# Kernel optimization log

Hardware: AMD Instinct MI355X
Metric: run time of the kernel (lower is better)

## Reference

```python
import jax, jax.numpy as jnp
import numpy as np

N_NODES = 50000
N_EDGES = 800000
N_GRAPHS = 64
IN_DIM, HID, OUT = 128, 128, 16


def gcn_conv(x, src, dst, deg_inv_sqrt, W, b):
    # x: [N, Cin]; src/dst: [E+N] (self-loops appended); W: [Cin, Cout]
    h = x @ W                                   # [N, Cout]
    norm = deg_inv_sqrt[src] * deg_inv_sqrt[dst]  # [E+N]
    msg = h[src] * norm[:, None]                # gather + scale
    out = jax.ops.segment_sum(msg, dst, num_segments=N_NODES)
    return out + b


def setup_inputs() -> dict:
    key = jax.random.key(0)
    ks = jax.random.split(key, 8)
    x = jax.random.normal(ks[0], (N_NODES, IN_DIM), dtype=jnp.float32)
    edge_index = jax.random.randint(ks[1], (2, N_EDGES), 0, N_NODES, dtype=jnp.int64)
    batch = jnp.sort(jax.random.randint(ks[2], (N_NODES,), 0, N_GRAPHS, dtype=jnp.int64))
    s = 1.0 / np.sqrt(IN_DIM)
    W1 = jax.random.normal(ks[3], (IN_DIM, HID), dtype=jnp.float32) * s
    b1 = jnp.zeros((HID,), dtype=jnp.float32)
    W2 = jax.random.normal(ks[4], (HID, HID), dtype=jnp.float32) * (1.0 / np.sqrt(HID))
    b2 = jnp.zeros((HID,), dtype=jnp.float32)
    Wfc = jax.random.normal(ks[5], (HID, OUT), dtype=jnp.float32) * (1.0 / np.sqrt(HID))
    bfc = jnp.zeros((OUT,), dtype=jnp.float32)
    return {"x": x, "edge_index": edge_index, "batch": batch,
            "W1": W1, "b1": b1, "W2": W2, "b2": b2, "Wfc": Wfc, "bfc": bfc}


def reference(x, edge_index, batch, W1, b1, W2, b2, Wfc, bfc):
    self_loops = jnp.arange(N_NODES, dtype=edge_index.dtype)
    src = jnp.concatenate([edge_index[0], self_loops])  # [E+N]
    dst = jnp.concatenate([edge_index[1], self_loops])
    deg = jax.ops.segment_sum(jnp.ones_like(dst, dtype=x.dtype), dst, num_segments=N_NODES)
    deg_inv_sqrt = jnp.where(deg > 0, jax.lax.rsqrt(deg), 0.0)

    h = jax.nn.relu(gcn_conv(x, src, dst, deg_inv_sqrt, W1, b1))
    h = jax.nn.relu(gcn_conv(h, src, dst, deg_inv_sqrt, W2, b2))

    # global mean pool over graphs
    sums = jax.ops.segment_sum(h, batch, num_segments=N_GRAPHS)         # [G, HID]
    cnts = jax.ops.segment_sum(jnp.ones((N_NODES,), h.dtype), batch, num_segments=N_GRAPHS)
    pooled = sums / jnp.maximum(cnts, 1.0)[:, None]

    return pooled @ Wfc + bfc  # [G, OUT]
```

## Files before the change

### kernel.cpp

```cpp
#include <hip/hip_runtime.h>
#include <math.h>

#define N_NODES 50000
#define N_EDGES 800000
#define N_GRAPHS 64
#define DIM 128
#define OUTD 16

#define BSHIFT 8
#define BNODES 256
#define NBUCK ((N_NODES + BNODES - 1) / BNODES)
#define TILE 2048
#define RCAP 8192
#define BSLOT 4864
#define GEMMB 256
#define BIN_GRID ((N_EDGES + TILE - 1) / TILE)

typedef __attribute__((ext_vector_type(8))) short short8;
typedef __attribute__((ext_vector_type(4))) float f32x4;

static __device__ __forceinline__ unsigned short f2bf(float f) {
    unsigned u = __float_as_uint(f);
    u += 0x7fffu + ((u >> 16) & 1u);
    return (unsigned short)(u >> 16);
}
static __device__ __forceinline__ float bfl(unsigned u) {
    return __uint_as_float(u << 16);
}
static __device__ __forceinline__ float bfh(unsigned u) {
    return __uint_as_float(u & 0xffff0000u);
}

__global__ __launch_bounds__(256) void k_init(int* __restrict__ bcnt,
                                              float* __restrict__ pool,
                                              const float* __restrict__ W2,
                                              unsigned* __restrict__ W2f) {
    int tid = threadIdx.x;
    if (tid < NBUCK) bcnt[tid] = 0;
    for (int i = tid; i < N_GRAPHS * DIM; i += 256) pool[i] = 0.f;
    for (int idx = tid; idx < (DIM / 2) * DIM; idx += 256) {
        int kp = idx >> 7;
        int n  = idx & 127;
        int k  = kp * 2;
        int kstep = kp >> 4;
        int quad  = (kp >> 2) & 3;
        int jw    = kp & 3;
        int ct    = n >> 4;
        unsigned vlo = f2bf(W2[(size_t)k * DIM + n]);
        unsigned vhi = f2bf(W2[(size_t)(k + 1) * DIM + n]);
        W2f[(((kstep * 8 + ct) * 64) + quad * 16 + (n & 15)) * 4 + jw] = vlo | (vhi << 16);
    }
}

template <int BF16IN>
static __device__ __forceinline__ void gemm_body(const void* __restrict__ Av,
                                                 const float* __restrict__ Wg,
                                                 unsigned short* __restrict__ C,
                                                 int nrows,
                                                 unsigned* smemW, unsigned* smemC,
                                                 int tile0, int tstride) {
    unsigned* Wl = smemW;
    {
        int t = threadIdx.x;
        int p = t & 63;
        int kp = p * 2;
        int n0 = (t >> 6) * 32;
        int kstep = kp >> 5;
        int quad = (kp >> 3) & 3;
        int jw = (kp & 7) >> 1;
        const float* r0 = Wg + (size_t)kp * DIM;
        const float* r1 = r0 + DIM;
        int rot = (p >> 2) & 7;
#pragma unroll
        for (int i4 = 0; i4 < 8; ++i4) {
            int nb = ((i4 + rot) & 7) * 4;
            int n = n0 + nb;
            float4 lo = *(const float4*)(r0 + n);
            float4 hi = *(const float4*)(r1 + n);
            const float* lp = &lo.x;
            const float* hp = &hi.x;
#pragma unroll
            for (int ii = 0; ii < 4; ++ii) {
                int nn = n + ii;
                int ct = nn >> 4;
                int l  = quad * 16 + (nn & 15);
                unsigned vlo = f2bf(lp[ii]);
                unsigned vhi = f2bf(hp[ii]);
                Wl[(((kstep * 8 + ct) * 64) + l) * 4 + jw] = vlo | (vhi << 16);
            }
        }
    }
    __syncthreads();

    int wid  = threadIdx.x >> 6;
    int lane = threadIdx.x & 63;
    int m    = lane & 15;
    int quad = lane >> 4;
    const short8* Wf = (const short8*)Wl;
    unsigned short* cs = (unsigned short*)smemC + wid * 4352;
    const unsigned char* cb = (const unsigned char*)smemC + wid * 8704;

    int ntiles = (nrows + 127) / 128;
    for (int tile = tile0; tile < ntiles; tile += tstride) {
        int row0 = tile * 128 + wid * 32;
        if (row0 >= nrows) continue;

        int rA = row0 + m;      if (rA >= nrows) rA = nrows - 1;
        int rB = row0 + 16 + m; if (rB >= nrows) rB = nrows - 1;

        short8 af0[4], af1[4];
        if (BF16IN) {
            const unsigned short* arowA = (const unsigned short*)Av + (size_t)rA * DIM + quad * 8;
            const unsigned short* arowB = (const unsigned short*)Av + (size_t)rB * DIM + quad * 8;
#pragma unroll
            for (int ks = 0; ks < 4; ++ks) {
                af0[ks] = *(const short8*)(arowA + ks * 32);
                af1[ks] = *(const short8*)(arowB + ks * 32);
            }
        } else {
            const float* arowA = (const float*)Av + (size_t)rA * DIM + quad * 8;
            const float* arowB = (const float*)Av + (size_t)rB * DIM + quad * 8;
#pragma unroll
            for (int ks = 0; ks < 4; ++ks) {
                float4 lo = *(const float4*)(arowA + ks * 32);
                float4 hi = *(const float4*)(arowA + ks * 32 + 4);
                short8 f;
                f[0] = (short)f2bf(lo.x); f[1] = (short)f2bf(lo.y);
                f[2] = (short)f2bf(lo.z); f[3] = (short)f2bf(lo.w);
                f[4] = (short)f2bf(hi.x); f[5] = (short)f2bf(hi.y);
                f[6] = (short)f2bf(hi.z); f[7] = (short)f2bf(hi.w);
                af0[ks] = f;
                lo = *(const float4*)(arowB + ks * 32);
                hi = *(const float4*)(arowB + ks * 32 + 4);
                f[0] = (short)f2bf(lo.x); f[1] = (short)f2bf(lo.y);
                f[2] = (short)f2bf(lo.z); f[3] = (short)f2bf(lo.w);
                f[4] = (short)f2bf(hi.x); f[5] = (short)f2bf(hi.y);
                f[6] = (short)f2bf(hi.z); f[7] = (short)f2bf(hi.w);
                af1[ks] = f;
            }
        }

        f32x4 acc0[8], acc1[8];
#pragma unroll
        for (int ct = 0; ct < 8; ++ct) {
            acc0[ct] = (f32x4){0.f, 0.f, 0.f, 0.f};
            acc1[ct] = (f32x4){0.f, 0.f, 0.f, 0.f};
        }

#pragma unroll
        for (int ks = 0; ks < 4; ++ks) {
#pragma unroll
            for (int ct = 0; ct < 8; ++ct) {
                short8 bfrag = Wf[(ks * 8 + ct) * 64 + lane];
                acc0[ct] = __builtin_amdgcn_mfma_f32_16x16x32_bf16(af0[ks], bfrag, acc0[ct], 0, 0, 0);
                acc1[ct] = __builtin_amdgcn_mfma_f32_16x16x32_bf16(af1[ks], bfrag, acc1[ct], 0, 0, 0);
            }
        }

#pragma unroll
        for (int ct = 0; ct < 8; ++ct) {
#pragma unroll
            for (int reg = 0; reg < 4; ++reg) {
                cs[(quad * 4 + reg) * 136 + ct * 16 + m]      = f2bf(acc0[ct][reg]);
                cs[(16 + quad * 4 + reg) * 136 + ct * 16 + m] = f2bf(acc1[ct][reg]);
            }
        }
#pragma unroll
        for (int i = 0; i < 8; ++i) {
            int rg = i * 4 + quad;
            int r = row0 + rg;
            if (r < nrows) {
                uint4 vv = *(const uint4*)(cb + rg * 272 + m * 16);
                *((uint4*)(C + (size_t)r * DIM) + m) = vv;
            }
        }
    }
}

__global__ __launch_bounds__(256) void k_fused1(const float* __restrict__ A,
                                                const float* __restrict__ Wg,
                                                unsigned short* __restrict__ C,
                                                int nrows,
                                                const int* __restrict__ src,
                                                const int* __restrict__ dstp,
                                                int* __restrict__ bcnt,
                                                unsigned* __restrict__ bucket_arr) {
    __shared__ unsigned smemW[32768 / 4];
    __shared__ unsigned smemC[34816 / 4];
    if (blockIdx.x >= GEMMB) {
        int* cnt  = (int*)smemW;
        int* base = cnt + NBUCK;
        int tile0 = (blockIdx.x - GEMMB) * TILE;
        for (int i = threadIdx.x; i < NBUCK; i += 256) cnt[i] = 0;
        __syncthreads();
#pragma unroll
        for (int j = 0; j < TILE / 512; ++j) {
            int e = tile0 + j * 512 + threadIdx.x * 2;
            if (e < N_EDGES) {
                int2 d = *(const int2*)(dstp + e);
                atomicAdd(&cnt[d.x >> BSHIFT], 1);
                atomicAdd(&cnt[d.y >> BSHIFT], 1);
            }
        }
        __syncthreads();
        for (int i = threadIdx.x; i < NBUCK; i += 256) {
            int c = cnt[i];
            base[i] = i * BSLOT + (c ? atomicAdd(&bcnt[i], c) : 0);
            cnt[i] = 0;
        }
        __syncthreads();
#pragma unroll
        for (int j = 0; j < TILE / 512; ++j) {
            int e = tile0 + j * 512 + threadIdx.x * 2;
            if (e < N_EDGES) {
                int2 s = *(const int2*)(src + e);
                int2 d = *(const int2*)(dstp + e);
                int b0 = d.x >> BSHIFT, b1 = d.y >> BSHIFT;
                int p0 = base[b0] + atomicAdd(&cnt[b0], 1);
                bucket_arr[p0] = (unsigned)s.x | ((unsigned)(d.x & 255) << 16);
                int p1 = base[b1] + atomicAdd(&cnt[b1], 1);
                bucket_arr[p1] = (unsigned)s.y | ((unsigned)(d.y & 255) << 16);
            }
        }
        return;
    }
    gemm_body<0>(A, Wg, C, nrows, smemW, smemC, blockIdx.x, GEMMB);
}

__global__ __launch_bounds__(256) void k_binB(const unsigned* __restrict__ barr,
                                              const int* __restrict__ bcnt,
                                              int* __restrict__ row_off,
                                              float* __restrict__ dis,
                                              unsigned short* __restrict__ csr,
                                              unsigned* __restrict__ Hw) {
    __shared__ unsigned raw[RCAP];
    __shared__ unsigned short stage[RCAP];
    __shared__ int hist[BNODES];
    __shared__ int scn[BNODES];
    __shared__ int borig[256], bscan[256];
    __shared__ float sdis[256];
    int tid = threadIdx.x;
    int b = blockIdx.x;
    int n0 = b << BSHIFT;

    int cv = (tid < NBUCK) ? bcnt[tid] : 0;
    borig[tid] = cv;
    bscan[tid] = cv;
    __syncthreads();
    for (int off = 1; off < 256; off <<= 1) {
        int t = (tid >= off) ? bscan[tid - off] : 0;
        __syncthreads();
        bscan[tid] += t;
        __syncthreads();
    }
    int rbase = bscan[b] - borig[b];
    int len = borig[b];
    const unsigned* bin = barr + (size_t)b * BSLOT;

    hist[tid] = 0;
    __syncthreads();
    for (int i = tid; i < len; i += 256) {
        unsigned ed = bin[i];
        if (i < RCAP) raw[i] = ed;
        atomicAdd(&hist[ed >> 16], 1);
    }
    __syncthreads();
    int v = hist[tid];
    scn[tid] = v;
    __syncthreads();
    for (int off = 1; off < 256; off <<= 1) {
        int t = (tid >= off) ? scn[tid - off] : 0;
        __syncthreads();
        scn[tid] += t;
        __syncthreads();
    }
    int excl = scn[tid] - v;
    int n = n0 + tid;
    float dv = rsqrtf((float)(v + 1));
    sdis[tid] = dv;
    if (n < N_NODES) {
        row_off[n] = rbase + excl;
        dis[n] = dv;
    }
    if (b == NBUCK - 1 && tid == 0) row_off[N_NODES] = N_EDGES;
    hist[tid] = excl;
    __syncthreads();
    for (int i = tid; i < len; i += 256) {
        unsigned ed = (i < RCAP) ? raw[i] : bin[i];
        int p = atomicAdd(&hist[ed >> 16], 1);
        unsigned short sv = (unsigned short)(ed & 0xffffu);
        if (p < RCAP) stage[p] = sv;
        else csr[rbase + p] = sv;
    }
    __syncthreads();
    int lim = min(len, RCAP);
    for (int i = tid; i < lim; i += 256)
        csr[rbase + i] = stage[i];

    int nrows_b = min(N_NODES - n0, 256);
    uint4* Hv = (uint4*)(Hw + ((size_t)n0 << 6));
    int nvec = nrows_b * 16;
    for (int i = tid; i < nvec; i += 256) {
        int r = i >> 4;
        float ds = sdis[r];
        uint4 u = Hv[i];
        u.x = (unsigned)f2bf(bfl(u.x) * ds) | ((unsigned)f2bf(bfh(u.x) * ds) << 16);
        u.y = (unsigned)f2bf(bfl(u.y) * ds) | ((unsigned)f2bf(bfh(u.y) * ds) << 16);
        u.z = (unsigned)f2bf(bfl(u.z) * ds) | ((unsigned)f2bf(bfh(u.z) * ds) << 16);
        u.w = (unsigned)f2bf(bfl(u.w) * ds) | ((unsigned)f2bf(bfh(u.w) * ds) << 16);
        Hv[i] = u;
    }
}

template <int MODE>
__global__ __launch_bounds__(256) void k_agg(const uint4* __restrict__ Hb4,
                                             const int* __restrict__ row_off,
                                             const unsigned short* __restrict__ csr,
                                             const float* __restrict__ dis,
                                             const float* __restrict__ bias,
                                             uint4* __restrict__ out,
                                             const int* __restrict__ batch,
                                             float* __restrict__ pool,
                                             const short8* __restrict__ W2f) {
    __shared__ unsigned char smem[8768];
    __shared__ float sdS[16];
    int lane = threadIdx.x & 15;
    int nl   = threadIdx.x >> 4;
    int node = blockIdx.x * 16 + nl;

    float dn = dis[node];
    if (lane == 0) sdS[nl] = dn;
    uint4 hp = Hb4[(size_t)node * 16 + lane];
    float a0[8], a1[8], a2[8], a3[8];
    a0[0] = bfl(hp.x); a0[1] = bfh(hp.x);
    a0[2] = bfl(hp.y); a0[3] = bfh(hp.y);
    a0[4] = bfl(hp.z); a0[5] = bfh(hp.z);
    a0[6] = bfl(hp.w); a0[7] = bfh(hp.w);
#pragma unroll
    for (int j = 0; j < 8; ++j) { a1[j] = 0.f; a2[j] = 0.f; a3[j] = 0.f; }

#define ACC8(A, g) do { \
        A[0] += bfl(g.x); A[1] += bfh(g.x); \
        A[2] += bfl(g.y); A[3] += bfh(g.y); \
        A[4] += bfl(g.z); A[5] += bfh(g.z); \
        A[6] += bfl(g.w); A[7] += bfh(g.w); \
    } while (0)

    int e = row_off[node], e1 = row_off[node + 1];
    for (; e + 8 <= e1; e += 8) {
        int s0 = csr[e];     int s1 = csr[e + 1];
        int s2 = csr[e + 2]; int s3 = csr[e + 3];
        int s4 = csr[e + 4]; int s5 = csr[e + 5];
        int s6 = csr[e + 6]; int s7 = csr[e + 7];
        uint4 g0 = Hb4[(size_t)s0 * 16 + lane];
        uint4 g1 = Hb4[(size_t)s1 * 16 + lane];
        uint4 g2 = Hb4[(size_t)s2 * 16 + lane];
        uint4 g3 = Hb4[(size_t)s3 * 16 + lane];
        uint4 g4 = Hb4[(size_t)s4 * 16 + lane];
        uint4 g5 = Hb4[(size_t)s5 * 16 + lane];
        uint4 g6 = Hb4[(size_t)s6 * 16 + lane];
        uint4 g7 = Hb4[(size_t)s7 * 16 + lane];
        ACC8(a0, g0); ACC8(a1, g1); ACC8(a2, g2); ACC8(a3, g3);
        ACC8(a0, g4); ACC8(a1, g5); ACC8(a2, g6); ACC8(a3, g7);
    }
    for (; e + 4 <= e1; e += 4) {
        int s0 = csr[e];     int s1 = csr[e + 1];
        int s2 = csr[e + 2]; int s3 = csr[e + 3];
        uint4 g0 = Hb4[(size_t)s0 * 16 + lane];
        uint4 g1 = Hb4[(size_t)s1 * 16 + lane];
        uint4 g2 = Hb4[(size_t)s2 * 16 + lane];
        uint4 g3 = Hb4[(size_t)s3 * 16 + lane];
        ACC8(a0, g0); ACC8(a1, g1); ACC8(a2, g2); ACC8(a3, g3);
    }
    for (; e < e1; ++e) {
        int s = csr[e];
        uint4 g = Hb4[(size_t)s * 16 + lane];
        ACC8(a0, g);
    }
#undef ACC8

    float4 b0 = ((const float4*)bias)[lane * 2];
    float4 b1v = ((const float4*)bias)[lane * 2 + 1];
    float r[8];
    r[0] = fmaxf(fmaf(dn, a0[0] + a1[0] + a2[0] + a3[0], b0.x), 0.f);
    r[1] = fmaxf(fmaf(dn, a0[1] + a1[1] + a2[1] + a3[1], b0.y), 0.f);
    r[2] = fmaxf(fmaf(dn, a0[2] + a1[2] + a2[2] + a3[2], b0.z), 0.f);
    r[3] = fmaxf(fmaf(dn, a0[3] + a1[3] + a2[3] + a3[3], b0.w), 0.f);
    r[4] = fmaxf(fmaf(dn, a0[4] + a1[4] + a2[4] + a3[4], b1v.x), 0.f);
    r[5] = fmaxf(fmaf(dn, a0[5] + a1[5] + a2[5] + a3[5], b1v.y), 0.f);
    r[6] = fmaxf(fmaf(dn, a0[6] + a1[6] + a2[6] + a3[6], b1v.z), 0.f);
    r[7] = fmaxf(fmaf(dn, a0[7] + a1[7] + a2[7] + a3[7], b1v.w), 0.f);

    if (MODE == 2) {
        unsigned short* sA = (unsigned short*)smem;
        unsigned short* sC = (unsigned short*)smem + 2176;
        uint4 av;
        av.x = (unsigned)f2bf(r[0]) | ((unsigned)f2bf(r[1]) << 16);
        av.y = (unsigned)f2bf(r[2]) | ((unsigned)f2bf(r[3]) << 16);
        av.z = (unsigned)f2bf(r[4]) | ((unsigned)f2bf(r[5]) << 16);
        av.w = (unsigned)f2bf(r[6]) | ((unsigned)f2bf(r[7]) << 16);
        *(uint4*)(sA + nl * 136 + lane * 8) = av;
        __syncthreads();

        int wid = threadIdx.x >> 6;
        int l64 = threadIdx.x & 63;
        int m   = l64 & 15;
        int q   = l64 >> 4;
        short8 af[4];
#pragma unroll
        for (int ks = 0; ks < 4; ++ks)
            af[ks] = *(const short8*)(sA + m * 136 + ks * 32 + q * 8);
        f32x4 acc[2];
        acc[0] = (f32x4){0.f, 0.f, 0.f, 0.f};
        acc[1] = (f32x4){0.f, 0.f, 0.f, 0.f};
#pragma unroll
        for (int ks = 0; ks < 4; ++ks) {
#pragma unroll
            for (int j = 0; j < 2; ++j) {
                int ct = wid * 2 + j;
                short8 bfrag = W2f[(ks * 8 + ct) * 64 + l64];
                acc[j] = __builtin_amdgcn_mfma_f32_16x16x32_bf16(af[ks], bfrag, acc[j], 0, 0, 0);
            }
        }
#pragma unroll
        for (int j = 0; j < 2; ++j) {
#pragma unroll
            for (int reg = 0; reg < 4; ++reg) {
                float sc = sdS[q * 4 + reg];
                sC[(q * 4 + reg) * 136 + (wid * 2 + j) * 16 + m] = f2bf(acc[j][reg] * sc);
            }
        }
        __syncthreads();
        {
            int t = threadIdx.x;
            int row = t >> 4, ch = t & 15;
            uint4 vv = *(const uint4*)((const unsigned char*)sC + row * 272 + ch * 16);
            out[(size_t)(blockIdx.x * 16 + row) * 16 + ch] = vv;
        }
    } else {
        float* sacc = (float*)smem;
        int* sg = (int*)(smem + 16 * DIM * 4);
#pragma unroll
        for (int j = 0; j < 8; ++j) sacc[nl * DIM + lane * 8 + j] = r[j];
        if (lane == 0) sg[nl] = batch[node];
        __syncthreads();
        int c = threadIdx.x;
        if (c < DIM) {
            float acc = 0.f;
            int curg = sg[0];
#pragma unroll
            for (int n2 = 0; n2 < 16; ++n2) {
                int g = sg[n2];
                if (g != curg) {
                    atomicAdd(&pool[curg * DIM + c], acc);
                    acc = 0.f; curg = g;
                }
                acc += sacc[n2 * DIM + c];
            }
            atomicAdd(&pool[curg * DIM + c], acc);
        }
    }
}

__global__ void k_fc(const float* __restrict__ pool, const int* __restrict__ batch,
                     const float* __restrict__ Wfc, const float* __restrict__ bfc,
                     float* __restrict__ out) {
    int id = blockIdx.x * blockDim.x + threadIdx.x;
    if (id >= N_GRAPHS * OUTD) return;
    int g = id >> 4, o = id & 15;
    int lo = 0, hi = N_NODES;
    while (lo < hi) { int mid = (lo + hi) >> 1; if (batch[mid] < g) lo = mid + 1; else hi = mid; }
    int l0 = lo;
    lo = 0; hi = N_NODES;
    while (lo < hi) { int mid = (lo + hi) >> 1; if (batch[mid] < g + 1) lo = mid + 1; else hi = mid; }
    int cntg = lo - l0;
    float inv = 1.0f / fmaxf((float)cntg, 1.0f);
    float acc = bfc[o];
    const float* p = pool + g * DIM;
    for (int c = 0; c < DIM; ++c)
        acc = fmaf(p[c] * inv, Wfc[c * OUTD + o], acc);
    out[id] = acc;
}


extern "C" void kernel_launch(void* const* d_in, const int* in_sizes, int n_in,
                              void* d_out, int out_size, void* d_ws, size_t ws_size,
                              hipStream_t stream) {
    const float* x    = (const float*)d_in[0];
    const int*   ei   = (const int*)d_in[1];
    const int*   batch= (const int*)d_in[2];
    const float* W1   = (const float*)d_in[3];
    const float* b1   = (const float*)d_in[4];
    const float* W2   = (const float*)d_in[5];
    const float* b2   = (const float*)d_in[6];
    const float* Wfc  = (const float*)d_in[7];
    const float* bfc  = (const float*)d_in[8];
    float* out = (float*)d_out;

    char* ws = (char*)d_ws;
    size_t off = 0;
    auto alloc = [&](size_t bytes) -> char* {
        char* p = ws + off;
        off = (off + bytes + 255) & ~(size_t)255;
        return p;
    };
    int*      bcnt     = (int*)     alloc((size_t)NBUCK * 4);
    int*      row_off  = (int*)     alloc((size_t)(N_NODES + 1) * 4);
    float*    dis      = (float*)   alloc((size_t)N_NODES * 4);
    unsigned short* csr= (unsigned short*)alloc((size_t)N_EDGES * 2);
    unsigned* barr     = (unsigned*)alloc((size_t)NBUCK * BSLOT * 4);
    float*    pool     = (float*)   alloc((size_t)N_GRAPHS * DIM * 4);
    unsigned* W2f      = (unsigned*)alloc((size_t)(DIM / 2) * DIM * 4);
    unsigned short* Hb = (unsigned short*)alloc((size_t)N_NODES * DIM * 2);
    unsigned short* Hb2= (unsigned short*)alloc((size_t)N_NODES * DIM * 2);

    const int* src = ei;
    const int* dst = ei + N_EDGES;

    k_init<<<1, 256, 0, stream>>>(bcnt, pool, W2, W2f);
    k_fused1<<<GEMMB + BIN_GRID, 256, 0, stream>>>(x, W1, Hb, N_NODES,
                                                   src, dst, bcnt, barr);
    k_binB<<<NBUCK, 256, 0, stream>>>(barr, bcnt, row_off, dis, csr, (unsigned*)Hb);

    int agg_grid = (N_NODES + 15) / 16;
    k_agg<2><<<agg_grid, 256, 0, stream>>>((const uint4*)Hb, row_off, csr, dis, b1,
                                           (uint4*)Hb2, batch, pool, (const short8*)W2f);
    k_agg<1><<<agg_grid, 256, 0, stream>>>((const uint4*)Hb2, row_off, csr, dis, b2,
                                           nullptr, batch, pool, nullptr);
    k_fc<<<(N_GRAPHS * OUTD + 255) / 256, 256, 0, stream>>>(pool, batch, Wfc, bfc, out);
}
```

Before: 205.0 us.

## Sort nodes by degree within buckets to balance aggregation wavefronts

k_binB now bitonic-sorts each 256-node bucket by in-degree and writes a permutation. Both aggregation kernels process nodes in that order, so the 16 nodes in a block, and the nodes sharing a wavefront, have similar edge counts and less divergence. Output rows are scattered through the permutation. The pooling step now sorts the block's graph ids with an insertion sort on one thread so the run-length atomics stay correct. The 8-wide unrolled gather loop is also removed, which lowers the number of loads in flight per lane.

After: 221.5 us. +8.1%, slower.

```diff
diff --git a/kernel.cpp b/kernel.cpp
--- a/kernel.cpp
+++ b/kernel.cpp
@@ -232,13 +232,15 @@
                                               int* __restrict__ row_off,
                                               float* __restrict__ dis,
                                               unsigned short* __restrict__ csr,
-                                              unsigned* __restrict__ Hw) {
+                                              unsigned* __restrict__ Hw,
+                                              int* __restrict__ perm) {
     __shared__ unsigned raw[RCAP];
     __shared__ unsigned short stage[RCAP];
     __shared__ int hist[BNODES];
     __shared__ int scn[BNODES];
     __shared__ int borig[256], bscan[256];
     __shared__ float sdis[256];
+    __shared__ int skey[256];
     int tid = threadIdx.x;
     int b = blockIdx.x;
     int n0 = b << BSHIFT;
@@ -276,6 +278,7 @@
     }
     int excl = scn[tid] - v;
     int n = n0 + tid;
+    int nrows_b = min(N_NODES - n0, 256);
     float dv = rsqrtf((float)(v + 1));
     sdis[tid] = dv;
     if (n < N_NODES) {
@@ -284,6 +287,8 @@
     }
     if (b == NBUCK - 1 && tid == 0) row_off[N_NODES] = N_EDGES;
     hist[tid] = excl;
+
+    skey[tid] = (n < N_NODES) ? ((v << 8) | tid) : (0x40000000 | tid);
     __syncthreads();
     for (int i = tid; i < len; i += 256) {
         unsigned ed = (i < RCAP) ? raw[i] : bin[i];
@@ -297,7 +302,23 @@
     for (int i = tid; i < lim; i += 256)
         csr[rbase + i] = stage[i];
 
-    int nrows_b = min(N_NODES - n0, 256);
+    for (int k = 2; k <= 256; k <<= 1) {
+        for (int j = k >> 1; j > 0; j >>= 1) {
+            __syncthreads();
+            int ixj = tid ^ j;
+            int a = skey[tid];
+            int p2 = skey[ixj];
+            bool up = ((tid & k) == 0);
+            int res;
+            if (ixj > tid) res = up ? min(a, p2) : max(a, p2);
+            else           res = up ? max(a, p2) : min(a, p2);
+            __syncthreads();
+            skey[tid] = res;
+        }
+    }
+    __syncthreads();
+    if (tid < nrows_b) perm[n0 + tid] = n0 + (skey[tid] & 255);
+
     uint4* Hv = (uint4*)(Hw + ((size_t)n0 << 6));
     int nvec = nrows_b * 16;
     for (int i = tid; i < nvec; i += 256) {
@@ -321,15 +342,18 @@
                                              uint4* __restrict__ out,
                                              const int* __restrict__ batch,
                                              float* __restrict__ pool,
-                                             const short8* __restrict__ W2f) {
+                                             const short8* __restrict__ W2f,
+                                             const int* __restrict__ perm) {
     __shared__ unsigned char smem[8768];
     __shared__ float sdS[16];
+    __shared__ int   spm[16];
+    __shared__ int   sidx[16];
     int lane = threadIdx.x & 15;
     int nl   = threadIdx.x >> 4;
-    int node = blockIdx.x * 16 + nl;
+    int node = perm[blockIdx.x * 16 + nl];
 
     float dn = dis[node];
-    if (lane == 0) sdS[nl] = dn;
+    if (lane == 0) { sdS[nl] = dn; spm[nl] = node; }
     uint4 hp = Hb4[(size_t)node * 16 + lane];
     float a0[8], a1[8], a2[8], a3[8];
     a0[0] = bfl(hp.x); a0[1] = bfh(hp.x);
@@ -347,22 +371,6 @@
     } while (0)
 
     int e = row_off[node], e1 = row_off[node + 1];
-    for (; e + 8 <= e1; e += 8) {
-        int s0 = csr[e];     int s1 = csr[e + 1];
-        int s2 = csr[e + 2]; int s3 = csr[e + 3];
-        int s4 = csr[e + 4]; int s5 = csr[e + 5];
-        int s6 = csr[e + 6]; int s7 = csr[e + 7];
-        uint4 g0 = Hb4[(size_t)s0 * 16 + lane];
-        uint4 g1 = Hb4[(size_t)s1 * 16 + lane];
-        uint4 g2 = Hb4[(size_t)s2 * 16 + lane];
-        uint4 g3 = Hb4[(size_t)s3 * 16 + lane];
-        uint4 g4 = Hb4[(size_t)s4 * 16 + lane];
-        uint4 g5 = Hb4[(size_t)s5 * 16 + lane];
-        uint4 g6 = Hb4[(size_t)s6 * 16 + lane];
-        uint4 g7 = Hb4[(size_t)s7 * 16 + lane];
-        ACC8(a0, g0); ACC8(a1, g1); ACC8(a2, g2); ACC8(a3, g3);
-        ACC8(a0, g4); ACC8(a1, g5); ACC8(a2, g6); ACC8(a3, g7);
-    }
     for (; e + 4 <= e1; e += 4) {
         int s0 = csr[e];     int s1 = csr[e + 1];
         int s2 = csr[e + 2]; int s3 = csr[e + 3];
@@ -435,7 +443,7 @@
             int t = threadIdx.x;
             int row = t >> 4, ch = t & 15;
             uint4 vv = *(const uint4*)((const unsigned char*)sC + row * 272 + ch * 16);
-            out[(size_t)(blockIdx.x * 16 + row) * 16 + ch] = vv;
+            out[(size_t)spm[row] * 16 + ch] = vv;
         }
     } else {
         float* sacc = (float*)smem;
@@ -444,18 +452,32 @@
         for (int j = 0; j < 8; ++j) sacc[nl * DIM + lane * 8 + j] = r[j];
         if (lane == 0) sg[nl] = batch[node];
         __syncthreads();
+        if (threadIdx.x == 0) {
+            int idx[16];
+#pragma unroll
+            for (int i = 0; i < 16; ++i) idx[i] = i;
+            for (int i = 1; i < 16; ++i) {
+                int t = idx[i]; int gv = sg[t]; int j2 = i - 1;
+                while (j2 >= 0 && sg[idx[j2]] > gv) { idx[j2 + 1] = idx[j2]; --j2; }
+                idx[j2 + 1] = t;
+            }
+#pragma unroll
+            for (int i = 0; i < 16; ++i) sidx[i] = idx[i];
+        }
+        __syncthreads();
         int c = threadIdx.x;
         if (c < DIM) {
             float acc = 0.f;
-            int curg = sg[0];
+            int curg = sg[sidx[0]];
 #pragma unroll
             for (int n2 = 0; n2 < 16; ++n2) {
-                int g = sg[n2];
+                int id2 = sidx[n2];
+                int g = sg[id2];
                 if (g != curg) {
                     atomicAdd(&pool[curg * DIM + c], acc);
                     acc = 0.f; curg = g;
                 }
-                acc += sacc[n2 * DIM + c];
+                acc += sacc[id2 * DIM + c];
             }
             atomicAdd(&pool[curg * DIM + c], acc);
         }
@@ -507,6 +529,7 @@
     int*      bcnt     = (int*)     alloc((size_t)NBUCK * 4);
     int*      row_off  = (int*)     alloc((size_t)(N_NODES + 1) * 4);
     float*    dis      = (float*)   alloc((size_t)N_NODES * 4);
+    int*      perm     = (int*)     alloc((size_t)N_NODES * 4);
     unsigned short* csr= (unsigned short*)alloc((size_t)N_EDGES * 2);
     unsigned* barr     = (unsigned*)alloc((size_t)NBUCK * BSLOT * 4);
     float*    pool     = (float*)   alloc((size_t)N_GRAPHS * DIM * 4);
@@ -520,12 +543,14 @@
     k_init<<<1, 256, 0, stream>>>(bcnt, pool, W2, W2f);
     k_fused1<<<GEMMB + BIN_GRID, 256, 0, stream>>>(x, W1, Hb, N_NODES,
                                                    src, dst, bcnt, barr);
-    k_binB<<<NBUCK, 256, 0, stream>>>(barr, bcnt, row_off, dis, csr, (unsigned*)Hb);
+    k_binB<<<NBUCK, 256, 0, stream>>>(barr, bcnt, row_off, dis, csr,
+                                      (unsigned*)Hb, perm);
 
     int agg_grid = (N_NODES + 15) / 16;
     k_agg<2><<<agg_grid, 256, 0, stream>>>((const uint4*)Hb, row_off, csr, dis, b1,
-                                           (uint4*)Hb2, batch, pool, (const short8*)W2f);
+                                           (uint4*)Hb2, batch, pool,
+                                           (const short8*)W2f, perm);
     k_agg<1><<<agg_grid, 256, 0, stream>>>((const uint4*)Hb2, row_off, csr, dis, b2,
-                                           nullptr, batch, pool, nullptr);
+                                           nullptr, batch, pool, nullptr, perm);
     k_fc<<<(N_GRAPHS * OUTD + 255) / 256, 256, 0, stream>>>(pool, batch, Wfc, bfc, out);
 }
```
